# Kernel optimization log

Hardware: AMD Instinct MI355X
Metric: run time of the kernel (lower is better)

Reference implementation:

```python
import jax, jax.numpy as jnp
import numpy as np

B, S, D = 2, 2048, 1024
H, DH = 16, 64
N_CTX = 2048
IGNORE = -100000.0


def setup_inputs() -> dict:
    key = jax.random.key(0)
    ks = jax.random.split(key, 6)
    scale = 0.02
    return {
        "x": jax.random.normal(ks[0], (B, S, D), dtype=jnp.float32),
        "W_Q": jax.random.normal(ks[1], (H, DH, D), dtype=jnp.float32) * scale,
        "W_K": jax.random.normal(ks[2], (H, DH, D), dtype=jnp.float32) * scale,
        "W_V": jax.random.normal(ks[3], (H, DH, D), dtype=jnp.float32) * scale,
        "W_O": jax.random.normal(ks[4], (H, D, DH), dtype=jnp.float32) * scale,
        "b_Q": jnp.zeros((H, DH), dtype=jnp.float32),
        "b_K": jnp.zeros((H, DH), dtype=jnp.float32),
        "b_V": jnp.zeros((H, DH), dtype=jnp.float32),
        "b_O": jnp.zeros((D,), dtype=jnp.float32),
    }


def reference(x, W_Q, W_K, W_V, W_O, b_Q, b_K, b_V, b_O):
    attn_scale = jnp.sqrt(jnp.asarray(DH, dtype=x.dtype))
    # q,k,v: [batch, pos, head, d_head]
    q = jnp.einsum('ihm,bpm->bpih', W_Q, x) + b_Q
    k = jnp.einsum('ihm,bpm->bpih', W_K, x) + b_K
    v = jnp.einsum('ihm,bpm->bpih', W_V, x) + b_V
    # scores: [batch, head, q_pos, k_pos]
    attn_scores = jnp.einsum('bpih,bqih->bipq', q, k) / attn_scale
    # causal mask (pos_start=0, no kv cache)
    qs, ks_ = attn_scores.shape[-2], attn_scores.shape[-1]
    mask = jnp.tril(jnp.ones((qs, ks_), dtype=bool))
    attn_scores = jnp.where(mask, attn_scores, jnp.asarray(IGNORE, dtype=attn_scores.dtype))
    attn_matrix = jax.nn.softmax(attn_scores, axis=-1)
    # z: [batch, q_pos, head, d_head]
    z = jnp.einsum('bpih,biqp->bqih', v, attn_matrix)
    out = jnp.einsum('idh,bqih->bqd', W_O, z) + b_O
    return out
```

## Files before the change

### kernel.cpp

```cpp
#include <hip/hip_runtime.h>

typedef __bf16 bf16;
typedef __bf16 bf16x4 __attribute__((ext_vector_type(4)));
typedef __bf16 bf16x8 __attribute__((ext_vector_type(8)));
typedef float f32x4 __attribute__((ext_vector_type(4)));
typedef unsigned u32x4 __attribute__((ext_vector_type(4)));

#define AS1C(p) ((const __attribute__((address_space(1))) void*)(p))
#define AS3(p)  ((__attribute__((address_space(3))) void*)(p))

__device__ __forceinline__ void gld16(const bf16* gsrc, bf16* ldst) {
  __builtin_amdgcn_global_load_lds(AS1C(gsrc), AS3(ldst), 16, 0, 0);
}


__global__ void castx_kernel(const float* __restrict__ x, bf16* __restrict__ xb) {
  const int n4 = (4096 * 1024) / 4;
  for (int i = blockIdx.x * blockDim.x + threadIdx.x; i < n4; i += gridDim.x * blockDim.x) {
    float4 v = ((const float4*)x)[i];
    bf16x4 o;
    o[0] = (bf16)v.x; o[1] = (bf16)v.y; o[2] = (bf16)v.z; o[3] = (bf16)v.w;
    ((bf16x4*)xb)[i] = o;
  }
}

__global__ void prep_kernel(const float* __restrict__ WQ, const float* __restrict__ WK,
                            const float* __restrict__ WV, const float* __restrict__ WO,
                            const float* __restrict__ bQ, const float* __restrict__ bK,
                            const float* __restrict__ bV,
                            bf16* __restrict__ Wqkv, bf16* __restrict__ Wo2,
                            float* __restrict__ biasq) {
  const int WN = 1024 * 1024;
  const int total = 4 * WN + 3072;
  for (int i = blockIdx.x * blockDim.x + threadIdx.x; i < total; i += gridDim.x * blockDim.x) {
    if (i < WN) {
      Wqkv[i] = (bf16)(WQ[i] * 0.125f);
    } else if (i < 2 * WN) {
      Wqkv[i] = (bf16)WK[i - WN];
    } else if (i < 3 * WN) {
      Wqkv[i] = (bf16)WV[i - 2 * WN];
    } else if (i < 4 * WN) {
      int j = i - 3 * WN;
      int hh = j >> 16, r = j & 65535, d = r >> 6, dh = r & 63;
      Wo2[d * 1024 + hh * 64 + dh] = (bf16)WO[j];
    } else {
      int n = i - 4 * WN;
      biasq[n] = (n < 1024) ? bQ[n] * 0.125f : (n < 2048) ? bK[n - 1024] : bV[n - 2048];
    }
  }
}

template <int MODE>
__global__ __launch_bounds__(256, 2)
void gemm_bt(const bf16* __restrict__ A, const bf16* __restrict__ Bw,
             const float* __restrict__ bias,
             bf16* __restrict__ Qo, bf16* __restrict__ Ko, bf16* __restrict__ Vt,
             float* __restrict__ Co, int M, int N, int K) {
  __shared__ bf16 As[2][8192];
  __shared__ bf16 Bs[2][8192];
  const int tid = threadIdx.x;
  const int lane = tid & 63, w = tid >> 6;
  const int wr = w >> 1, wc = w & 1;
  const int g = lane >> 4, lr = lane & 15;
  const int perx = gridDim.x >> 3;
  const int tile = (blockIdx.x & 7) * perx + (blockIdx.x >> 3);
  const int brow = (tile & 31) * 128, bcol = (tile >> 5) * 128;

  auto stage = [&](int k0, int bufi) {
#pragma unroll
    for (int it = 0; it < 4; ++it) {
      const int cb = (it * 4 + w) * 64;
      const int u = cb + lane;
      const int lc = u ^ ((u >> 3) & 7);
      const int row = lc >> 3, c8 = (lc & 7) * 8;
      gld16(A + (size_t)(brow + row) * K + k0 + c8, &As[bufi][cb * 8]);
      gld16(Bw + (size_t)(bcol + row) * K + k0 + c8, &Bs[bufi][cb * 8]);
    }
  };

  f32x4 acc[4][4] = {};
  stage(0, 0);
  const int nstep = K >> 6;

  for (int t = 0; t < nstep; ++t) {
    __syncthreads();
    if (t + 1 < nstep) stage((t + 1) << 6, (t + 1) & 1);
    const bf16* as = As[t & 1];
    const bf16* bs = Bs[t & 1];
#pragma unroll
    for (int kk = 0; kk < 2; ++kk) {
      bf16x8 af[4], bfm[4];
#pragma unroll
      for (int m = 0; m < 4; ++m) {
        const int row = wr * 64 + m * 16 + lr;
        const int sl = (row * 8 + kk * 4 + g) ^ (lr & 7);
        af[m] = *(const bf16x8*)(as + sl * 8);
      }
#pragma unroll
      for (int n = 0; n < 4; ++n) {
        const int row = wc * 64 + n * 16 + lr;
        const int sl = (row * 8 + kk * 4 + g) ^ (lr & 7);
        bfm[n] = *(const bf16x8*)(bs + sl * 8);
      }
#pragma unroll
      for (int m = 0; m < 4; ++m)
#pragma unroll
        for (int n = 0; n < 4; ++n)
          acc[m][n] = __builtin_amdgcn_mfma_f32_16x16x32_bf16(af[m], bfm[n], acc[m][n], 0, 0, 0);
    }
  }

  const int row0 = brow + wr * 64;
  const int col0 = bcol + wc * 64;
#pragma unroll
  for (int m = 0; m < 4; ++m) {
#pragma unroll
    for (int n = 0; n < 4; ++n) {
      const int nidx = col0 + n * 16 + lr;
      f32x4 v = acc[m][n];
      const float bs = bias[nidx];
      if (MODE == 0) {
        const int stream = nidx >> 10;
        const int j = nidx & 1023;
        const int hh = j >> 6, dh = j & 63;
        const int r0 = row0 + m * 16 + g * 4;
        const int b = r0 >> 11;
        const int p0 = r0 & 2047;
        if (stream == 2) {
          bf16x4 vv;
#pragma unroll
          for (int i = 0; i < 4; ++i) vv[i] = (bf16)(v[i] + bs);
          *(bf16x4*)(Vt + ((size_t)(b * 16 + hh) * 64 + dh) * 2048 + p0) = vv;
        } else {
          bf16* dst = (stream == 0) ? Qo : Ko;
#pragma unroll
          for (int i = 0; i < 4; ++i)
            dst[((size_t)(b * 16 + hh) * 2048 + (p0 + i)) * 64 + dh] = (bf16)(v[i] + bs);
        }
      } else {
#pragma unroll
        for (int i = 0; i < 4; ++i) {
          const int r = row0 + m * 16 + g * 4 + i;
          Co[(size_t)r * 1024 + nidx] = v[i] + bs;
        }
      }
    }
  }
}

__global__ __launch_bounds__(256, 4)
void attn_kernel(const bf16* __restrict__ Qm, const bf16* __restrict__ Km,
                 const bf16* __restrict__ Vm, bf16* __restrict__ Z,
                 bf16* __restrict__ OP, float2* __restrict__ ML) {
  const int nblk = blockIdx.x;
  const int xcd = nblk & 7, s2 = nblk >> 3;
  const int Gl = s2 & 3, u = s2 >> 2;
  const int G = Gl * 8 + xcd;
  const int hh = G & 15, b = G >> 4;
  const int lane = threadIdx.x & 63, w = threadIdx.x >> 6;
  const int g = lane >> 4, lr = lane & 15;
  const bool g0 = g & 1, g1 = (g >> 1) & 1;

  int qt, t0, t1, spl;
  if (u < 32) {
    qt = 31 - (u >> 1); spl = u & 1;
    const int T = qt + 1, mid = (T + 1) >> 1;
    t0 = spl ? mid : 0; t1 = spl ? T : mid;
  } else {
    qt = 47 - u; spl = -1; t0 = 0; t1 = qt + 1;
  }

  __shared__ bf16 Ks[2][4096];
  __shared__ bf16 Vs[2][4096];

  const bf16* Qb = Qm + (size_t)G * 2048 * 64;
  const bf16* Kb = Km + (size_t)G * 2048 * 64;
  const bf16* Vb = Vm + (size_t)G * 64 * 2048;

  auto stage = [&](int kv0, int bufi) {
#pragma unroll
    for (int it = 0; it < 2; ++it) {
      const int cb = w * 128 + it * 64;
      const int uu = cb + lane;
      const int lc = uu ^ ((uu >> 3) & 7);
      const int row = lc >> 3, c8 = (lc & 7) * 8;
      gld16(Kb + (size_t)(kv0 + row) * 64 + c8, &Ks[bufi][cb * 8]);
      gld16(Vb + (size_t)row * 2048 + kv0 + c8, &Vs[bufi][cb * 8]);
    }
  };

  const int q0w = qt * 64 + w * 16;
  const int qg = q0w + lr;

  bf16x8 aq[2];
#pragma unroll
  for (int kk = 0; kk < 2; ++kk)
    aq[kk] = *(const bf16x8*)(Qb + (size_t)qg * 64 + kk * 32 + g * 8);

  float m_i = -1e30f, l_i = 0.f;
  f32x4 oacc[4] = {};

  int buf = 0;
  stage(t0 * 64, 0);
  __syncthreads();

  for (int t = t0; t < t1; ++t) {
    if (t + 1 < t1) stage((t + 1) * 64, buf ^ 1);
    const int kv0 = t * 64;

    f32x4 s[4] = {};
#pragma unroll
    for (int kk = 0; kk < 2; ++kk) {
#pragma unroll
      for (int n = 0; n < 4; ++n) {
        const int r = n * 16 + lr;
        const int sl = (r * 8 + kk * 4 + g) ^ (r & 7);
        bf16x8 bk = *(const bf16x8*)(&Ks[buf][sl * 8]);
        s[n] = __builtin_amdgcn_mfma_f32_16x16x32_bf16(bk, aq[kk], s[n], 0, 0, 0);
      }
    }
    if (t == qt) {
#pragma unroll
      for (int n = 0; n < 4; ++n)
#pragma unroll
        for (int i = 0; i < 4; ++i)
          if (kv0 + n * 16 + g * 4 + i > qg) s[n][i] = -1e9f;
    }

    float tm = fmaxf(fmaxf(fmaxf(s[0][0], s[0][1]), fmaxf(s[0][2], s[0][3])),
                     fmaxf(fmaxf(s[1][0], s[1][1]), fmaxf(s[1][2], s[1][3])));
    tm = fmaxf(tm, fmaxf(fmaxf(fmaxf(s[2][0], s[2][1]), fmaxf(s[2][2], s[2][3])),
                         fmaxf(fmaxf(s[3][0], s[3][1]), fmaxf(s[3][2], s[3][3]))));
    tm = fmaxf(tm, __shfl_xor(tm, 16));
    tm = fmaxf(tm, __shfl_xor(tm, 32));
    const float mn = fmaxf(m_i, tm);
    const float al = __expf(m_i - mn);
    m_i = mn;
#pragma unroll
    for (int n = 0; n < 4; ++n)
#pragma unroll
      for (int i = 0; i < 4; ++i) s[n][i] = __expf(s[n][i] - mn);
    float ts = ((s[0][0] + s[0][1]) + (s[0][2] + s[0][3])) +
               ((s[1][0] + s[1][1]) + (s[1][2] + s[1][3])) +
               ((s[2][0] + s[2][1]) + (s[2][2] + s[2][3])) +
               ((s[3][0] + s[3][1]) + (s[3][2] + s[3][3]));
    ts += __shfl_xor(ts, 16);
    ts += __shfl_xor(ts, 32);
    l_i = l_i * al + ts;
#pragma unroll
    for (int n = 0; n < 4; ++n)
#pragma unroll
      for (int i = 0; i < 4; ++i) oacc[n][i] *= al;

    unsigned U[8];
#pragma unroll
    for (int n = 0; n < 4; ++n)
#pragma unroll
      for (int h = 0; h < 2; ++h) {
        unsigned lo = (unsigned)__builtin_bit_cast(unsigned short, (bf16)s[n][2 * h]);
        unsigned hi = (unsigned)__builtin_bit_cast(unsigned short, (bf16)s[n][2 * h + 1]);
        U[n * 2 + h] = lo | (hi << 16);
      }
    unsigned rA0 = (unsigned)__shfl_xor((int)(g1 ? U[0] : U[2]), 32);
    unsigned rA1 = (unsigned)__shfl_xor((int)(g1 ? U[1] : U[3]), 32);
    unsigned rA2 = (unsigned)__shfl_xor((int)(g1 ? U[4] : U[6]), 32);
    unsigned rA3 = (unsigned)__shfl_xor((int)(g1 ? U[5] : U[7]), 32);
    unsigned v2_000 = g1 ? rA0 : U[0];
    unsigned v2_001 = g1 ? rA1 : U[1];
    unsigned v2_010 = g1 ? U[2] : rA0;
    unsigned v2_011 = g1 ? U[3] : rA1;
    unsigned v2_100 = g1 ? rA2 : U[4];
    unsigned v2_101 = g1 ? rA3 : U[5];
    unsigned v2_110 = g1 ? U[6] : rA2;
    unsigned v2_111 = g1 ? U[7] : rA3;
    unsigned rB0 = (unsigned)__shfl_xor((int)(g0 ? v2_000 : v2_010), 16);
    unsigned rB1 = (unsigned)__shfl_xor((int)(g0 ? v2_001 : v2_011), 16);
    unsigned rB2 = (unsigned)__shfl_xor((int)(g0 ? v2_100 : v2_110), 16);
    unsigned rB3 = (unsigned)__shfl_xor((int)(g0 ? v2_101 : v2_111), 16);
    u32x4 t0v, t1v;
    t0v[0] = g0 ? rB0 : v2_000;
    t0v[1] = g0 ? rB1 : v2_001;
    t0v[2] = g0 ? v2_010 : rB0;
    t0v[3] = g0 ? v2_011 : rB1;
    t1v[0] = g0 ? rB2 : v2_100;
    t1v[1] = g0 ? rB3 : v2_101;
    t1v[2] = g0 ? v2_110 : rB2;
    t1v[3] = g0 ? v2_111 : rB3;
    bf16x8 pb0 = __builtin_bit_cast(bf16x8, t0v);
    bf16x8 pb1 = __builtin_bit_cast(bf16x8, t1v);

#pragma unroll
    for (int kk = 0; kk < 2; ++kk) {
      const bf16x8 pb = kk ? pb1 : pb0;
#pragma unroll
      for (int n = 0; n < 4; ++n) {
        const int r = n * 16 + lr;
        const int sl = (r * 8 + kk * 4 + g) ^ (r & 7);
        bf16x8 av = *(const bf16x8*)(&Vs[buf][sl * 8]);
        oacc[n] = __builtin_amdgcn_mfma_f32_16x16x32_bf16(av, pb, oacc[n], 0, 0, 0);
      }
    }
    __syncthreads();
    buf ^= 1;
  }

  if (u < 32) {
    const int pr = G * 1024 + (qt - 16) * 64 + w * 16 + lr;
    bf16* oprow = OP + (size_t)(spl * 32768 + pr) * 64;
#pragma unroll
    for (int n = 0; n < 4; ++n) {
      bf16x4 o4;
#pragma unroll
      for (int i = 0; i < 4; ++i) o4[i] = (bf16)oacc[n][i];
      *(bf16x4*)(oprow + n * 16 + g * 4) = o4;
    }
    if (lane < 16) ML[spl * 32768 + pr] = make_float2(m_i, l_i);
  } else {
    const float li = 1.f / l_i;
    bf16* zrow = Z + ((size_t)(b * 2048 + qg) * 16 + hh) * 64;
#pragma unroll
    for (int n = 0; n < 4; ++n) {
      bf16x4 o4;
#pragma unroll
      for (int i = 0; i < 4; ++i) o4[i] = (bf16)(oacc[n][i] * li);
      *(bf16x4*)(zrow + n * 16 + g * 4) = o4;
    }
  }
}

__global__ __launch_bounds__(256)
void combine_kernel(const bf16* __restrict__ OP, const float2* __restrict__ ML,
                    bf16* __restrict__ Z) {
  const int id = blockIdx.x * 256 + threadIdx.x;
  const int pr = id >> 3, d8 = id & 7;
  const float2 ml0 = ML[pr], ml1 = ML[32768 + pr];
  const float m = fmaxf(ml0.x, ml1.x);
  const float w0 = __expf(ml0.x - m), w1 = __expf(ml1.x - m);
  const float inv = 1.f / (ml0.y * w0 + ml1.y * w1);
  const bf16x8 a = *(const bf16x8*)(OP + (size_t)pr * 64 + d8 * 8);
  const bf16x8 c = *(const bf16x8*)(OP + ((size_t)32768 + pr) * 64 + d8 * 8);
  bf16x8 o;
#pragma unroll
  for (int j = 0; j < 8; ++j)
    o[j] = (bf16)(((float)a[j] * w0 + (float)c[j] * w1) * inv);
  const int bh = pr >> 10, qr = pr & 1023;
  const int bb = bh >> 4, hq = bh & 15;
  *(bf16x8*)(Z + (((size_t)(bb * 2048 + 1024 + qr)) * 16 + hq) * 64 + d8 * 8) = o;
}

extern "C" void kernel_launch(void* const* d_in, const int* in_sizes, int n_in,
                              void* d_out, int out_size, void* d_ws, size_t ws_size,
                              hipStream_t stream) {
  const float* x  = (const float*)d_in[0];
  const float* WQ = (const float*)d_in[1];
  const float* WK = (const float*)d_in[2];
  const float* WV = (const float*)d_in[3];
  const float* WO = (const float*)d_in[4];
  const float* bQ = (const float*)d_in[5];
  const float* bK = (const float*)d_in[6];
  const float* bV = (const float*)d_in[7];
  const float* bO = (const float*)d_in[8];
  float* out = (float*)d_out;

  char* ws = (char*)d_ws;
  bf16* xb    = (bf16*)(ws);
  bf16* Wqkv  = (bf16*)(ws + (8u << 20));
  bf16* Wo2   = (bf16*)(ws + (14u << 20));
  bf16* Qb    = (bf16*)(ws + (16u << 20));
  bf16* Kb    = (bf16*)(ws + (24u << 20));
  bf16* Vtb   = (bf16*)(ws + (32u << 20));
  bf16* Zb    = (bf16*)(ws + (40u << 20));
  float* biasq = (float*)(ws + (48u << 20));
  bf16* OP    = (bf16*)(ws);
  float2* ML  = (float2*)(ws + (8u << 20));

  castx_kernel<<<2048, 256, 0, stream>>>(x, xb);
  prep_kernel<<<2048, 256, 0, stream>>>(WQ, WK, WV, WO, bQ, bK, bV, Wqkv, Wo2, biasq);
  gemm_bt<0><<<768, 256, 0, stream>>>(xb, Wqkv, biasq, Qb, Kb, Vtb, nullptr,
                                      4096, 3072, 1024);
  attn_kernel<<<1536, 256, 0, stream>>>(Qb, Kb, Vtb, Zb, OP, ML);
  combine_kernel<<<1024, 256, 0, stream>>>(OP, ML, Zb);
  gemm_bt<1><<<256, 256, 0, stream>>>(Zb, Wo2, bO, nullptr, nullptr, nullptr, out,
                                      4096, 1024, 1024);
}
```

Baseline: 207.4 us.

## Fuse prep kernels, use exp2 softmax with lazy rescale and permlane swaps

Merges the x cast and weight prep into one launch, and folds log2(e) into the Q scale so softmax can use exp2f directly. The online-softmax rescale of the accumulator is skipped unless the running max grows by more than a threshold. The two xor shuffle stages that transpose P are replaced with permlane32/permlane16 swap builtins when the compiler provides them. These cut a launch, some exp and multiply work per tile, and cross-lane shuffle cost, at the risk of larger intermediate exponent values.

```diff
diff --git a/kernel.cpp b/kernel.cpp
--- a/kernel.cpp
+++ b/kernel.cpp
@@ -5,6 +5,7 @@
 typedef __bf16 bf16x8 __attribute__((ext_vector_type(8)));
 typedef float f32x4 __attribute__((ext_vector_type(4)));
 typedef unsigned u32x4 __attribute__((ext_vector_type(4)));
+typedef unsigned u32x2 __attribute__((ext_vector_type(2)));
 
 #define AS1C(p) ((const __attribute__((address_space(1))) void*)(p))
 #define AS3(p)  ((__attribute__((address_space(3))) void*)(p))
@@ -13,39 +14,40 @@
   __builtin_amdgcn_global_load_lds(AS1C(gsrc), AS3(ldst), 16, 0, 0);
 }
 
-
-__global__ void castx_kernel(const float* __restrict__ x, bf16* __restrict__ xb) {
-  const int n4 = (4096 * 1024) / 4;
-  for (int i = blockIdx.x * blockDim.x + threadIdx.x; i < n4; i += gridDim.x * blockDim.x) {
-    float4 v = ((const float4*)x)[i];
-    bf16x4 o;
-    o[0] = (bf16)v.x; o[1] = (bf16)v.y; o[2] = (bf16)v.z; o[3] = (bf16)v.w;
-    ((bf16x4*)xb)[i] = o;
-  }
-}
-
-__global__ void prep_kernel(const float* __restrict__ WQ, const float* __restrict__ WK,
-                            const float* __restrict__ WV, const float* __restrict__ WO,
-                            const float* __restrict__ bQ, const float* __restrict__ bK,
-                            const float* __restrict__ bV,
-                            bf16* __restrict__ Wqkv, bf16* __restrict__ Wo2,
-                            float* __restrict__ biasq) {
+#define QSCALE 0.18033688011112042f
+
+__global__ void prep_all(const float* __restrict__ x,
+                         const float* __restrict__ WQ, const float* __restrict__ WK,
+                         const float* __restrict__ WV, const float* __restrict__ WO,
+                         const float* __restrict__ bQ, const float* __restrict__ bK,
+                         const float* __restrict__ bV,
+                         bf16* __restrict__ xb, bf16* __restrict__ Wqkv,
+                         bf16* __restrict__ Wo2, float* __restrict__ biasq) {
+  const int X4 = (4096 * 1024) / 4;
   const int WN = 1024 * 1024;
-  const int total = 4 * WN + 3072;
+  const int total = X4 + 4 * WN + 3072;
   for (int i = blockIdx.x * blockDim.x + threadIdx.x; i < total; i += gridDim.x * blockDim.x) {
-    if (i < WN) {
-      Wqkv[i] = (bf16)(WQ[i] * 0.125f);
-    } else if (i < 2 * WN) {
-      Wqkv[i] = (bf16)WK[i - WN];
-    } else if (i < 3 * WN) {
-      Wqkv[i] = (bf16)WV[i - 2 * WN];
-    } else if (i < 4 * WN) {
-      int j = i - 3 * WN;
-      int hh = j >> 16, r = j & 65535, d = r >> 6, dh = r & 63;
-      Wo2[d * 1024 + hh * 64 + dh] = (bf16)WO[j];
+    if (i < X4) {
+      float4 v = ((const float4*)x)[i];
+      bf16x4 o;
+      o[0] = (bf16)v.x; o[1] = (bf16)v.y; o[2] = (bf16)v.z; o[3] = (bf16)v.w;
+      ((bf16x4*)xb)[i] = o;
     } else {
-      int n = i - 4 * WN;
-      biasq[n] = (n < 1024) ? bQ[n] * 0.125f : (n < 2048) ? bK[n - 1024] : bV[n - 2048];
+      int j = i - X4;
+      if (j < WN) {
+        Wqkv[j] = (bf16)(WQ[j] * QSCALE);
+      } else if (j < 2 * WN) {
+        Wqkv[j] = (bf16)WK[j - WN];
+      } else if (j < 3 * WN) {
+        Wqkv[j] = (bf16)WV[j - 2 * WN];
+      } else if (j < 4 * WN) {
+        int k = j - 3 * WN;
+        int hh = k >> 16, r = k & 65535, d = r >> 6, dh = r & 63;
+        Wo2[d * 1024 + hh * 64 + dh] = (bf16)WO[k];
+      } else {
+        int n = j - 4 * WN;
+        biasq[n] = (n < 1024) ? bQ[n] * QSCALE : (n < 2048) ? bK[n - 1024] : bV[n - 2048];
+      }
     }
   }
 }
@@ -233,24 +235,27 @@
                          fmaxf(fmaxf(s[3][0], s[3][1]), fmaxf(s[3][2], s[3][3]))));
     tm = fmaxf(tm, __shfl_xor(tm, 16));
     tm = fmaxf(tm, __shfl_xor(tm, 32));
-    const float mn = fmaxf(m_i, tm);
-    const float al = __expf(m_i - mn);
-    m_i = mn;
+    if (!__all(tm <= m_i + 12.f)) {
+      const float mn = fmaxf(m_i, tm);
+      const float al = exp2f(m_i - mn);
+      m_i = mn;
+      l_i *= al;
+#pragma unroll
+      for (int n = 0; n < 4; ++n)
+#pragma unroll
+        for (int i = 0; i < 4; ++i) oacc[n][i] *= al;
+    }
 #pragma unroll
     for (int n = 0; n < 4; ++n)
 #pragma unroll
-      for (int i = 0; i < 4; ++i) s[n][i] = __expf(s[n][i] - mn);
+      for (int i = 0; i < 4; ++i) s[n][i] = exp2f(s[n][i] - m_i);
     float ts = ((s[0][0] + s[0][1]) + (s[0][2] + s[0][3])) +
                ((s[1][0] + s[1][1]) + (s[1][2] + s[1][3])) +
                ((s[2][0] + s[2][1]) + (s[2][2] + s[2][3])) +
                ((s[3][0] + s[3][1]) + (s[3][2] + s[3][3]));
     ts += __shfl_xor(ts, 16);
     ts += __shfl_xor(ts, 32);
-    l_i = l_i * al + ts;
-#pragma unroll
-    for (int n = 0; n < 4; ++n)
-#pragma unroll
-      for (int i = 0; i < 4; ++i) oacc[n][i] *= al;
+    l_i += ts;
 
     unsigned U[8];
 #pragma unroll
@@ -261,31 +266,62 @@
         unsigned hi = (unsigned)__builtin_bit_cast(unsigned short, (bf16)s[n][2 * h + 1]);
         U[n * 2 + h] = lo | (hi << 16);
       }
-    unsigned rA0 = (unsigned)__shfl_xor((int)(g1 ? U[0] : U[2]), 32);
-    unsigned rA1 = (unsigned)__shfl_xor((int)(g1 ? U[1] : U[3]), 32);
-    unsigned rA2 = (unsigned)__shfl_xor((int)(g1 ? U[4] : U[6]), 32);
-    unsigned rA3 = (unsigned)__shfl_xor((int)(g1 ? U[5] : U[7]), 32);
-    unsigned v2_000 = g1 ? rA0 : U[0];
-    unsigned v2_001 = g1 ? rA1 : U[1];
-    unsigned v2_010 = g1 ? U[2] : rA0;
-    unsigned v2_011 = g1 ? U[3] : rA1;
-    unsigned v2_100 = g1 ? rA2 : U[4];
-    unsigned v2_101 = g1 ? rA3 : U[5];
-    unsigned v2_110 = g1 ? U[6] : rA2;
-    unsigned v2_111 = g1 ? U[7] : rA3;
-    unsigned rB0 = (unsigned)__shfl_xor((int)(g0 ? v2_000 : v2_010), 16);
-    unsigned rB1 = (unsigned)__shfl_xor((int)(g0 ? v2_001 : v2_011), 16);
-    unsigned rB2 = (unsigned)__shfl_xor((int)(g0 ? v2_100 : v2_110), 16);
-    unsigned rB3 = (unsigned)__shfl_xor((int)(g0 ? v2_101 : v2_111), 16);
+    unsigned v2_000, v2_001, v2_010, v2_011, v2_100, v2_101, v2_110, v2_111;
+#if __has_builtin(__builtin_amdgcn_permlane32_swap)
+    {
+      u32x2 pA0 = __builtin_amdgcn_permlane32_swap(U[0], U[2], false, false);
+      u32x2 pA1 = __builtin_amdgcn_permlane32_swap(U[1], U[3], false, false);
+      u32x2 pA2 = __builtin_amdgcn_permlane32_swap(U[4], U[6], false, false);
+      u32x2 pA3 = __builtin_amdgcn_permlane32_swap(U[5], U[7], false, false);
+      v2_000 = pA0[0]; v2_010 = pA0[1];
+      v2_001 = pA1[0]; v2_011 = pA1[1];
+      v2_100 = pA2[0]; v2_110 = pA2[1];
+      v2_101 = pA3[0]; v2_111 = pA3[1];
+    }
+#else
+    {
+      unsigned rA0 = (unsigned)__shfl_xor((int)(g1 ? U[0] : U[2]), 32);
+      unsigned rA1 = (unsigned)__shfl_xor((int)(g1 ? U[1] : U[3]), 32);
+      unsigned rA2 = (unsigned)__shfl_xor((int)(g1 ? U[4] : U[6]), 32);
+      unsigned rA3 = (unsigned)__shfl_xor((int)(g1 ? U[5] : U[7]), 32);
+      v2_000 = g1 ? rA0 : U[0];
+      v2_001 = g1 ? rA1 : U[1];
+      v2_010 = g1 ? U[2] : rA0;
+      v2_011 = g1 ? U[3] : rA1;
+      v2_100 = g1 ? rA2 : U[4];
+      v2_101 = g1 ? rA3 : U[5];
+      v2_110 = g1 ? U[6] : rA2;
+      v2_111 = g1 ? U[7] : rA3;
+    }
+#endif
     u32x4 t0v, t1v;
-    t0v[0] = g0 ? rB0 : v2_000;
-    t0v[1] = g0 ? rB1 : v2_001;
-    t0v[2] = g0 ? v2_010 : rB0;
-    t0v[3] = g0 ? v2_011 : rB1;
-    t1v[0] = g0 ? rB2 : v2_100;
-    t1v[1] = g0 ? rB3 : v2_101;
-    t1v[2] = g0 ? v2_110 : rB2;
-    t1v[3] = g0 ? v2_111 : rB3;
+#if __has_builtin(__builtin_amdgcn_permlane16_swap)
+    {
+      u32x2 pB0 = __builtin_amdgcn_permlane16_swap(v2_000, v2_010, false, false);
+      u32x2 pB1 = __builtin_amdgcn_permlane16_swap(v2_001, v2_011, false, false);
+      u32x2 pB2 = __builtin_amdgcn_permlane16_swap(v2_100, v2_110, false, false);
+      u32x2 pB3 = __builtin_amdgcn_permlane16_swap(v2_101, v2_111, false, false);
+      t0v[0] = pB0[0]; t0v[2] = pB0[1];
+      t0v[1] = pB1[0]; t0v[3] = pB1[1];
+      t1v[0] = pB2[0]; t1v[2] = pB2[1];
+      t1v[1] = pB3[0]; t1v[3] = pB3[1];
+    }
+#else
+    {
+      unsigned rB0 = (unsigned)__shfl_xor((int)(g0 ? v2_000 : v2_010), 16);
+      unsigned rB1 = (unsigned)__shfl_xor((int)(g0 ? v2_001 : v2_011), 16);
+      unsigned rB2 = (unsigned)__shfl_xor((int)(g0 ? v2_100 : v2_110), 16);
+      unsigned rB3 = (unsigned)__shfl_xor((int)(g0 ? v2_101 : v2_111), 16);
+      t0v[0] = g0 ? rB0 : v2_000;
+      t0v[1] = g0 ? rB1 : v2_001;
+      t0v[2] = g0 ? v2_010 : rB0;
+      t0v[3] = g0 ? v2_011 : rB1;
+      t1v[0] = g0 ? rB2 : v2_100;
+      t1v[1] = g0 ? rB3 : v2_101;
+      t1v[2] = g0 ? v2_110 : rB2;
+      t1v[3] = g0 ? v2_111 : rB3;
+    }
+#endif
     bf16x8 pb0 = __builtin_bit_cast(bf16x8, t0v);
     bf16x8 pb1 = __builtin_bit_cast(bf16x8, t1v);
 
@@ -335,7 +371,7 @@
   const int pr = id >> 3, d8 = id & 7;
   const float2 ml0 = ML[pr], ml1 = ML[32768 + pr];
   const float m = fmaxf(ml0.x, ml1.x);
-  const float w0 = __expf(ml0.x - m), w1 = __expf(ml1.x - m);
+  const float w0 = exp2f(ml0.x - m), w1 = exp2f(ml1.x - m);
   const float inv = 1.f / (ml0.y * w0 + ml1.y * w1);
   const bf16x8 a = *(const bf16x8*)(OP + (size_t)pr * 64 + d8 * 8);
   const bf16x8 c = *(const bf16x8*)(OP + ((size_t)32768 + pr) * 64 + d8 * 8);
@@ -374,8 +410,7 @@
   bf16* OP    = (bf16*)(ws);
   float2* ML  = (float2*)(ws + (8u << 20));
 
-  castx_kernel<<<2048, 256, 0, stream>>>(x, xb);
-  prep_kernel<<<2048, 256, 0, stream>>>(WQ, WK, WV, WO, bQ, bK, bV, Wqkv, Wo2, biasq);
+  prep_all<<<2048, 256, 0, stream>>>(x, WQ, WK, WV, WO, bQ, bK, bV, xb, Wqkv, Wo2, biasq);
   gemm_bt<0><<<768, 256, 0, stream>>>(xb, Wqkv, biasq, Qb, Kb, Vtb, nullptr,
                                       4096, 3072, 1024);
   attn_kernel<<<1536, 256, 0, stream>>>(Qb, Kb, Vtb, Zb, OP, ML);
```

Result: no change. 205.8 us (-0.7%).
